# Kernel tuning notes

Hardware: AMD Instinct MI355X
Metric: run time of the kernel (lower is better)

Reference implementation:

```python
import jax, jax.numpy as jnp
import numpy as np

H = 16
D_HEAD = 64  # model_dim // head_count = 1024 // 16
MODEL_DIM = 1024
MODEL_DIM1 = 768


def setup_inputs() -> dict:
    key = jax.random.key(0)
    ks = jax.random.split(key, 12)
    B, Q, K = 4, 1024, 1024
    inp = {
        "key": jax.random.normal(ks[0], (B, K, MODEL_DIM), jnp.float32),
        "value": jax.random.normal(ks[1], (B, K, MODEL_DIM), jnp.float32),
        "query": jax.random.normal(ks[2], (B, Q, MODEL_DIM1), jnp.float32),
        "mask": jax.random.randint(ks[3], (B, Q), 0, 2, jnp.int32),
        "additional_mask": jax.random.randint(ks[4], (B, K), 0, 2, jnp.int32),
        # learned params (nn.Linear weights stored as [in, out] for x @ W)
        "Wk": 0.02 * jax.random.normal(ks[5], (MODEL_DIM, H * D_HEAD), jnp.float32),
        "bk": jnp.zeros((H * D_HEAD,), jnp.float32),
        "Wv": 0.02 * jax.random.normal(ks[6], (MODEL_DIM, H * D_HEAD), jnp.float32),
        "bv": jnp.zeros((H * D_HEAD,), jnp.float32),
        "Wq": 0.02 * jax.random.normal(ks[7], (MODEL_DIM1, H * D_HEAD), jnp.float32),
        "bq": jnp.zeros((H * D_HEAD,), jnp.float32),
        "Wo": 0.02 * jax.random.normal(ks[8], (H * D_HEAD, MODEL_DIM1), jnp.float32),
        "bo": jnp.zeros((MODEL_DIM1,), jnp.float32),
    }
    return inp


def reference(key, value, query, mask, additional_mask, Wk, bk, Wv, bv, Wq, bq, Wo, bo):
    B, K_len = key.shape[0], key.shape[1]
    Q_len = query.shape[1]

    def shape(x):  # [B, L, H*d] -> [B, H, L, d]
        return x.reshape(B, -1, H, D_HEAD).transpose(0, 2, 1, 3)

    k = shape(key @ Wk + bk)
    v = shape(value @ Wv + bv)
    q = shape(query @ Wq + bq) / jnp.sqrt(jnp.float32(D_HEAD))

    scores = jnp.einsum("bhqd,bhkd->bhqk", q, k)  # [B,H,Q,K]
    top_score = scores[:, 0, :, :]  # pre-mask scores of head 0

    neg = jnp.float32(-1e18)
    scores = jnp.where(mask[:, None, :, None] == 0, neg, scores)
    scores = jnp.where(additional_mask[:, None, None, :] == 0, neg, scores)

    attn = jax.nn.softmax(scores, axis=-1)
    # dropout omitted (eval mode / deterministic reference)
    ctx = jnp.einsum("bhqk,bhkd->bhqd", attn, v)
    ctx = ctx.transpose(0, 2, 1, 3).reshape(B, Q_len, H * D_HEAD)
    output = ctx @ Wo + bo
    return output, top_score
```

## Files before the change

kernel.cpp:

```cpp
#include <hip/hip_runtime.h>
#include <hip/hip_bf16.h>

typedef __bf16 bf16_t;
typedef __bf16 bf16x8 __attribute__((ext_vector_type(8)));
typedef __bf16 bf16x4 __attribute__((ext_vector_type(4)));
typedef float  f32x4  __attribute__((ext_vector_type(4)));
typedef int    i32x4  __attribute__((ext_vector_type(4)));

#define MFMA16(a,b,c) __builtin_amdgcn_mfma_f32_16x16x32_bf16((a),(b),(c),0,0,0)

static constexpr int Bn = 4, Hn = 16, Dh = 64, SEQ = 1024;

__device__ __forceinline__ void gll16(const void* g, void* l) {
    __builtin_amdgcn_global_load_lds(
        (const __attribute__((address_space(1))) void*)g,
        (__attribute__((address_space(3))) void*)l, 16, 0, 0);
}

__global__ __launch_bounds__(256)
void wtrans_kernel(const float* __restrict__ s0, const float* __restrict__ s1,
                   const float* __restrict__ s2, const float* __restrict__ s3,
                   bf16_t* __restrict__ d0, bf16_t* __restrict__ d1,
                   bf16_t* __restrict__ d2, bf16_t* __restrict__ d3)
{
    __shared__ bf16_t tile[64][72];
    const int bid = blockIdx.x, t = threadIdx.x;
    const float* src; bf16_t* dst; int R, C, tr, tc;
    if (bid < 256)      { src = s0; dst = d0; R = 1024; C = 1024; tr = bid >> 4;        tc = bid & 15; }
    else if (bid < 512) { src = s1; dst = d1; R = 1024; C = 1024; tr = (bid-256) >> 4;  tc = (bid-256) & 15; }
    else if (bid < 704) { src = s2; dst = d2; R = 768;  C = 1024; tr = (bid-512) >> 4;  tc = (bid-512) & 15; }
    else                { src = s3; dst = d3; R = 1024; C = 768;  tr = (bid-704) / 12;  tc = (bid-704) % 12; }
    const int r0 = tr * 64, c0 = tc * 64;
    const int lr = t >> 2, lc0 = (t & 3) * 16;
    #pragma unroll
    for (int i = 0; i < 4; i++) {
        f32x4 v = *(const f32x4*)&src[(size_t)(r0 + lr) * C + c0 + lc0 + i * 4];
        #pragma unroll
        for (int j = 0; j < 4; j++) tile[lr][lc0 + i * 4 + j] = (bf16_t)v[j];
    }
    __syncthreads();
    const int oc = t >> 2, orc0 = (t & 3) * 16;
    #pragma unroll
    for (int i = 0; i < 2; i++) {
        bf16x8 vv;
        #pragma unroll
        for (int j = 0; j < 8; j++) vv[j] = tile[orc0 + i * 8 + j][oc];
        *(bf16x8*)&dst[(size_t)(c0 + oc) * R + r0 + orc0 + i * 8] = vv;
    }
}

template<int KD, int N, int MODE, typename AT>
__global__ __launch_bounds__(256)
void gemm_bt(const AT* __restrict__ A, const bf16_t* __restrict__ Bt,
             const float* __restrict__ bias, void* __restrict__ outp,
             float scale)
{
    __shared__ bf16_t As[2][128 * 32];
    __shared__ bf16_t Bs[2][64 * 32];
    __shared__ bf16_t Ct[(MODE == 2) ? 1 : 128 * 72];
    const int t = threadIdx.x, lane = t & 63, w = t >> 6;
    const int wr = w >> 1, wc = w & 1;
    const int row0 = blockIdx.y * 128, col0 = blockIdx.x * 64;
    const int lrow = lane & 15, lk4 = lane >> 4, lk8 = lk4 * 8;
    const int ar = t >> 1, ac = (t & 1) * 16;

    f32x4 acc[4][2] = {};
    f32x4 a_f[4];

    auto aload = [&](int kk) {
        if constexpr (sizeof(AT) == 4) {
            const float* src = (const float*)A + (size_t)(row0 + ar) * KD + kk + ac;
            a_f[0] = *(const f32x4*)(src);
            a_f[1] = *(const f32x4*)(src + 4);
            a_f[2] = *(const f32x4*)(src + 8);
            a_f[3] = *(const f32x4*)(src + 12);
        }
    };
    auto awrite = [&](int buf) {
        if constexpr (sizeof(AT) == 4) {
            bf16x8 v0, v1;
            #pragma unroll
            for (int j = 0; j < 4; j++) {
                v0[j] = (bf16_t)a_f[0][j]; v0[4 + j] = (bf16_t)a_f[1][j];
                v1[j] = (bf16_t)a_f[2][j]; v1[4 + j] = (bf16_t)a_f[3][j];
            }
            *(bf16x8*)&As[buf][ar * 32 + ac]     = v0;
            *(bf16x8*)&As[buf][ar * 32 + ac + 8] = v1;
        }
    };
    auto astage_gll = [&](int buf, int kk) {
        if constexpr (sizeof(AT) == 2) {
            #pragma unroll
            for (int j = 0; j < 2; j++) {
                const int idx = j * 256 + t;
                const bf16_t* g = (const bf16_t*)A +
                    (size_t)(row0 + (idx >> 2)) * KD + kk + (idx & 3) * 8;
                gll16(g, &As[buf][(j * 256 + w * 64) * 8]);
            }
        }
    };
    auto bstage = [&](int buf, int kk) {
        const bf16_t* g = Bt + (size_t)(col0 + (t >> 2)) * KD + kk + (t & 3) * 8;
        gll16(g, &Bs[buf][w * 512]);
    };

    constexpr int NB = KD / 32;
    if constexpr (sizeof(AT) == 4) { aload(0); awrite(0); }
    else                            astage_gll(0, 0);
    bstage(0, 0);

    for (int s = 0; s < NB; s++) {
        __syncthreads();
        const int cur = s & 1;
        if (s + 1 < NB) {
            bstage(cur ^ 1, (s + 1) * 32);
            if constexpr (sizeof(AT) == 4) aload((s + 1) * 32);
            else                           astage_gll(cur ^ 1, (s + 1) * 32);
        }
        bf16x8 af[4], bfr[2];
        #pragma unroll
        for (int mf = 0; mf < 4; mf++)
            af[mf] = *(const bf16x8*)&As[cur][(wr * 64 + mf * 16 + lrow) * 32 + lk8];
        #pragma unroll
        for (int nf = 0; nf < 2; nf++)
            bfr[nf] = *(const bf16x8*)&Bs[cur][(wc * 32 + nf * 16 + lrow) * 32 + lk8];
        #pragma unroll
        for (int mf = 0; mf < 4; mf++)
            #pragma unroll
            for (int nf = 0; nf < 2; nf++)
                acc[mf][nf] = MFMA16(af[mf], bfr[nf], acc[mf][nf]);
        if (s + 1 < NB) { if constexpr (sizeof(AT) == 4) awrite(cur ^ 1); }
    }

    if constexpr (MODE == 2) {
        #pragma unroll
        for (int mf = 0; mf < 4; mf++)
            #pragma unroll
            for (int nf = 0; nf < 2; nf++) {
                const int gcol = col0 + wc * 32 + nf * 16 + lrow;
                const float bv = bias[gcol];
                #pragma unroll
                for (int r = 0; r < 4; r++) {
                    const int grow = row0 + wr * 64 + mf * 16 + lk4 * 4 + r;
                    ((float*)outp)[(size_t)grow * N + gcol] = (acc[mf][nf][r] + bv) * scale;
                }
            }
    } else {
        __syncthreads();
        #pragma unroll
        for (int mf = 0; mf < 4; mf++)
            #pragma unroll
            for (int nf = 0; nf < 2; nf++) {
                const int lcol = wc * 32 + nf * 16 + lrow;
                const float bv = bias[col0 + lcol];
                #pragma unroll
                for (int r = 0; r < 4; r++)
                    Ct[(wr * 64 + mf * 16 + lk4 * 4 + r) * 72 + lcol] =
                        (bf16_t)((acc[mf][nf][r] + bv) * scale);
            }
        __syncthreads();
        const int h = col0 >> 6, b = row0 >> 10;
        bf16_t* op = (bf16_t*)outp + ((size_t)(b * Hn + h) << 16);
        if constexpr (MODE == 0) {
            #pragma unroll
            for (int j = 0; j < 4; j++) {
                const int sl = j * 32 + (t >> 3), cl0 = (t & 7) * 8;
                bf16x8 v = *(const bf16x8*)&Ct[sl * 72 + cl0];
                *(bf16x8*)&op[(size_t)((row0 & 1023) + sl) * 64 + cl0] = v;
            }
        } else {
            #pragma unroll
            for (int jj = 0; jj < 2; jj++) {
                const int cl = jj * 32 + (t >> 3);
                #pragma unroll
                for (int k = 0; k < 2; k++) {
                    const int sl0 = k * 64 + (t & 7) * 8;
                    bf16x8 v;
                    #pragma unroll
                    for (int i = 0; i < 8; i++) v[i] = Ct[(sl0 + i) * 72 + cl];
                    *(bf16x8*)&op[(size_t)cl * 1024 + (row0 & 1023) + sl0] = v;
                }
            }
        }
    }
}

__global__ __launch_bounds__(256)
void attn_kernel(const bf16_t* __restrict__ kbuf, const bf16_t* __restrict__ vT,
                 const bf16_t* __restrict__ qbuf, const int* __restrict__ qmask,
                 const int* __restrict__ kmask, bf16_t* __restrict__ ctx)
{
    __shared__ bf16_t Pall[4][16 * 64];
    const int t = threadIdx.x, lane = t & 63, w = t >> 6;
    const int bidx = blockIdx.x;
    const int qt = bidx & 15, bh = bidx >> 4, b = bh >> 4, h = bh & 15;
    const int lrow = lane & 15, lk4 = lane >> 4, lk8 = lk4 * 8;
    const int wrow0 = qt * 64 + w * 16;
    const bf16_t* kb = kbuf + (size_t)bh * SEQ * Dh;
    const bf16_t* vb = vT + (size_t)bh * Dh * SEQ;
    char* Pw = (char*)&Pall[w][0];
    const int sw = (lrow & 7) << 4;

    bf16x8 aq0, aq1;
    {
        const bf16_t* qp = qbuf + ((size_t)bh * SEQ + wrow0 + lrow) * Dh + lk8;
        aq0 = *(const bf16x8*)(qp);
        aq1 = *(const bf16x8*)(qp + 32);
    }
    const int qm = qmask[b * SEQ + wrow0 + lrow];

    float m_run = -__builtin_inff(), l_run = 0.f;
    f32x4 o[4] = {};

    bf16x8 kc0[4], kc1[4];
    #pragma unroll
    for (int nf = 0; nf < 4; nf++) {
        const bf16_t* kp = kb + (size_t)(nf * 16 + lrow) * Dh + lk8;
        kc0[nf] = *(const bf16x8*)(kp);
        kc1[nf] = *(const bf16x8*)(kp + 32);
    }

    for (int kt = 0; kt < 16; kt++) {
        const int key0 = kt * 64;
        bf16x8 vf0[4], vf1[4];
        #pragma unroll
        for (int nf = 0; nf < 4; nf++) {
            const bf16_t* vp = vb + (size_t)(nf * 16 + lrow) * SEQ + key0 + lk8;
            vf0[nf] = *(const bf16x8*)(vp);
            vf1[nf] = *(const bf16x8*)(vp + 32);
        }
        i32x4 km[4];
        #pragma unroll
        for (int nf = 0; nf < 4; nf++)
            km[nf] = *(const i32x4*)&kmask[b * SEQ + key0 + nf * 16 + lk4 * 4];
        f32x4 s4[4] = {};
        #pragma unroll
        for (int nf = 0; nf < 4; nf++) {
            s4[nf] = MFMA16(kc0[nf], aq0, s4[nf]);
            s4[nf] = MFMA16(kc1[nf], aq1, s4[nf]);
        }
        bf16x8 kn0[4], kn1[4];
        if (kt < 15) {
            #pragma unroll
            for (int nf = 0; nf < 4; nf++) {
                const bf16_t* kp = kb + (size_t)(key0 + 64 + nf * 16 + lrow) * Dh + lk8;
                kn0[nf] = *(const bf16x8*)(kp);
                kn1[nf] = *(const bf16x8*)(kp + 32);
            }
        }
        float p[4][4];
        float mt = m_run;
        #pragma unroll
        for (int nf = 0; nf < 4; nf++)
            #pragma unroll
            for (int r = 0; r < 4; r++) {
                const float sv = (qm && km[nf][r]) ? s4[nf][r] : -1e18f;
                p[nf][r] = sv;
                mt = fmaxf(mt, sv);
            }
        mt = fmaxf(mt, __shfl_xor(mt, 16));
        mt = fmaxf(mt, __shfl_xor(mt, 32));
        const float resc = __expf(m_run - mt);
        m_run = mt;
        float rs = 0.f;
        #pragma unroll
        for (int nf = 0; nf < 4; nf++)
            #pragma unroll
            for (int r = 0; r < 4; r++) {
                p[nf][r] = __expf(p[nf][r] - m_run);
                rs += p[nf][r];
            }
        rs += __shfl_xor(rs, 16);
        rs += __shfl_xor(rs, 32);
        l_run = l_run * resc + rs;
        #pragma unroll
        for (int nf = 0; nf < 4; nf++)
            #pragma unroll
            for (int r = 0; r < 4; r++) o[nf][r] *= resc;
        #pragma unroll
        for (int nf = 0; nf < 4; nf++) {
            bf16x4 pk;
            #pragma unroll
            for (int r = 0; r < 4; r++) pk[r] = (bf16_t)p[nf][r];
            *(bf16x4*)(Pw + lrow * 128 + ((nf * 32 + lk4 * 8) ^ sw)) = pk;
        }
        bf16x8 pa0 = *(const bf16x8*)(Pw + lrow * 128 + ((lk4 * 16) ^ sw));
        bf16x8 pa1 = *(const bf16x8*)(Pw + lrow * 128 + ((64 + lk4 * 16) ^ sw));
        #pragma unroll
        for (int nf = 0; nf < 4; nf++) {
            o[nf] = MFMA16(vf0[nf], pa0, o[nf]);
            o[nf] = MFMA16(vf1[nf], pa1, o[nf]);
        }
        #pragma unroll
        for (int nf = 0; nf < 4; nf++) { kc0[nf] = kn0[nf]; kc1[nf] = kn1[nf]; }
    }
    const float inv = 1.0f / l_run;
    #pragma unroll
    for (int nf = 0; nf < 4; nf++) {
        bf16x4 pk;
        #pragma unroll
        for (int r = 0; r < 4; r++) pk[r] = (bf16_t)(o[nf][r] * inv);
        *(bf16x4*)(Pw + lrow * 128 + ((nf * 32 + lk4 * 8) ^ sw)) = pk;
    }
    const int qp2 = lane >> 2, ch = lane & 3;
    const int sw2 = (qp2 & 7) << 4;
    bf16x8 o0 = *(const bf16x8*)(Pw + qp2 * 128 + ((ch * 32) ^ sw2));
    bf16x8 o1 = *(const bf16x8*)(Pw + qp2 * 128 + ((ch * 32 + 16) ^ sw2));
    bf16_t* cp = ctx + ((size_t)(b * SEQ + wrow0 + qp2)) * 1024 + h * 64 + ch * 16;
    *(bf16x8*)cp = o0;
    *(bf16x8*)(cp + 8) = o1;
}

__global__ __launch_bounds__(256)
void topsc_kernel(const bf16_t* __restrict__ kbuf, const bf16_t* __restrict__ qbuf,
                  float* __restrict__ topsc)
{
    const int t = threadIdx.x, lane = t & 63, w = t >> 6;
    const int bx = blockIdx.x;
    const int b = bx >> 6, qt = (bx >> 2) & 15, kq = bx & 3;
    const int lrow = lane & 15, lk4 = lane >> 4, lk8 = lk4 * 8;
    const int wrow0 = qt * 64 + w * 16;
    const bf16_t* kb = kbuf + ((size_t)(b * Hn)) * SEQ * Dh;
    const bf16_t* qp = qbuf + ((size_t)(b * Hn)) * SEQ * Dh
                     + (size_t)(wrow0 + lrow) * Dh + lk8;
    bf16x8 aq0 = *(const bf16x8*)(qp);
    bf16x8 aq1 = *(const bf16x8*)(qp + 32);
    for (int kt = 0; kt < 4; kt++) {
        const int key0 = kq * 256 + kt * 64;
        f32x4 s4[4] = {};
        #pragma unroll
        for (int nf = 0; nf < 4; nf++) {
            const bf16_t* kp = kb + (size_t)(key0 + nf * 16 + lrow) * Dh + lk8;
            s4[nf] = MFMA16(aq0, *(const bf16x8*)(kp), s4[nf]);
            s4[nf] = MFMA16(aq1, *(const bf16x8*)(kp + 32), s4[nf]);
        }
        #pragma unroll
        for (int nf = 0; nf < 4; nf++)
            #pragma unroll
            for (int r = 0; r < 4; r++)
                topsc[(size_t)(b * SEQ + wrow0 + lk4 * 4 + r) * SEQ +
                      key0 + nf * 16 + lrow] = s4[nf][r];
    }
}

extern "C" void kernel_launch(void* const* d_in, const int* in_sizes, int n_in,
                              void* d_out, int out_size, void* d_ws, size_t ws_size,
                              hipStream_t stream)
{
    const float* key   = (const float*)d_in[0];
    const float* value = (const float*)d_in[1];
    const float* query = (const float*)d_in[2];
    const int*   mask  = (const int*)d_in[3];
    const int*   amask = (const int*)d_in[4];
    const float* Wk = (const float*)d_in[5];
    const float* bk = (const float*)d_in[6];
    const float* Wv = (const float*)d_in[7];
    const float* bv = (const float*)d_in[8];
    const float* Wq = (const float*)d_in[9];
    const float* bq = (const float*)d_in[10];
    const float* Wo = (const float*)d_in[11];
    const float* bo = (const float*)d_in[12];

    const size_t per = (size_t)Bn * Hn * SEQ * Dh;
    bf16_t* kproj = (bf16_t*)d_ws;
    bf16_t* vT    = kproj + per;
    bf16_t* qproj = vT + per;
    bf16_t* ctx   = qproj + per;

    float* outf = (float*)d_out;
    bf16_t* WkT = (bf16_t*)(outf + (size_t)Bn * SEQ * 768);
    bf16_t* WvT = WkT + 1024 * 1024;
    bf16_t* WqT = WvT + 1024 * 1024;
    bf16_t* WoT = WqT + 1024 * 768;
    float* topsc = outf + (size_t)Bn * SEQ * 768;

    wtrans_kernel<<<896, 256, 0, stream>>>(Wk, Wv, Wq, Wo, WkT, WvT, WqT, WoT);
    gemm_bt<1024, 1024, 0, float><<<dim3(16, 32), 256, 0, stream>>>(key,   WkT, bk, kproj, 1.0f);
    gemm_bt<1024, 1024, 1, float><<<dim3(16, 32), 256, 0, stream>>>(value, WvT, bv, vT,    1.0f);
    gemm_bt< 768, 1024, 0, float><<<dim3(16, 32), 256, 0, stream>>>(query, WqT, bq, qproj, 0.125f);
    attn_kernel<<<dim3(Bn * Hn * 16), 256, 0, stream>>>(kproj, vT, qproj, mask, amask, ctx);
    gemm_bt<1024, 768, 2, bf16_t><<<dim3(12, 32), 256, 0, stream>>>(ctx, WoT, bo, outf, 1.0f);
    topsc_kernel<<<256, 256, 0, stream>>>(kproj, qproj, topsc);
}
```

Before: 369.2 us.

## Widen GEMM K-step with swizzled LDS; lazy rescale and MFMA row-sum in attention

The projection GEMM now stages 64-wide K slices instead of 32, using an XOR-swizzled LDS layout, so there are half as many barrier iterations and fewer bank conflicts. The attention kernel skips the online-softmax rescale unless the running max grows by more than a threshold. It also computes the row sum with an extra MFMA against a ones vector instead of shuffle reductions, and raises wave priority around MFMA blocks. This uses more LDS and registers and may lower occupancy, and the bf16 row sum adds some rounding error.

```diff
diff --git a/kernel.cpp b/kernel.cpp
--- a/kernel.cpp
+++ b/kernel.cpp
@@ -55,80 +55,102 @@
              const float* __restrict__ bias, void* __restrict__ outp,
              float scale)
 {
-    __shared__ bf16_t As[2][128 * 32];
-    __shared__ bf16_t Bs[2][64 * 32];
+    __shared__ bf16_t As[2][128 * 64];
+    __shared__ bf16_t Bs[2][64 * 64];
     __shared__ bf16_t Ct[(MODE == 2) ? 1 : 128 * 72];
     const int t = threadIdx.x, lane = t & 63, w = t >> 6;
     const int wr = w >> 1, wc = w & 1;
     const int row0 = blockIdx.y * 128, col0 = blockIdx.x * 64;
     const int lrow = lane & 15, lk4 = lane >> 4, lk8 = lk4 * 8;
-    const int ar = t >> 1, ac = (t & 1) * 16;
+    const int ar = t >> 1, ac0 = (t & 1) * 32;
 
     f32x4 acc[4][2] = {};
-    f32x4 a_f[4];
+    f32x4 a_f[8];
 
     auto aload = [&](int kk) {
         if constexpr (sizeof(AT) == 4) {
-            const float* src = (const float*)A + (size_t)(row0 + ar) * KD + kk + ac;
-            a_f[0] = *(const f32x4*)(src);
-            a_f[1] = *(const f32x4*)(src + 4);
-            a_f[2] = *(const f32x4*)(src + 8);
-            a_f[3] = *(const f32x4*)(src + 12);
+            const float* src = (const float*)A + (size_t)(row0 + ar) * KD + kk + ac0;
+            #pragma unroll
+            for (int j = 0; j < 8; j++) a_f[j] = *(const f32x4*)(src + j * 4);
         }
     };
     auto awrite = [&](int buf) {
         if constexpr (sizeof(AT) == 4) {
-            bf16x8 v0, v1;
+            char* base = (char*)&As[buf][0] + ar * 128;
+            const int aswz = (ar & 7) << 4;
             #pragma unroll
             for (int j = 0; j < 4; j++) {
-                v0[j] = (bf16_t)a_f[0][j]; v0[4 + j] = (bf16_t)a_f[1][j];
-                v1[j] = (bf16_t)a_f[2][j]; v1[4 + j] = (bf16_t)a_f[3][j];
-            }
-            *(bf16x8*)&As[buf][ar * 32 + ac]     = v0;
-            *(bf16x8*)&As[buf][ar * 32 + ac + 8] = v1;
+                bf16x8 v;
+                #pragma unroll
+                for (int e = 0; e < 4; e++) {
+                    v[e]     = (bf16_t)a_f[2 * j][e];
+                    v[4 + e] = (bf16_t)a_f[2 * j + 1][e];
+                }
+                *(bf16x8*)(base + ((ac0 * 2 + j * 16) ^ aswz)) = v;
+            }
         }
     };
     auto astage_gll = [&](int buf, int kk) {
         if constexpr (sizeof(AT) == 2) {
             #pragma unroll
-            for (int j = 0; j < 2; j++) {
+            for (int j = 0; j < 4; j++) {
                 const int idx = j * 256 + t;
-                const bf16_t* g = (const bf16_t*)A +
-                    (size_t)(row0 + (idx >> 2)) * KD + kk + (idx & 3) * 8;
-                gll16(g, &As[buf][(j * 256 + w * 64) * 8]);
+                const int row = idx >> 3, colb = (idx & 7) * 16;
+                const bf16_t* g = (const bf16_t*)A + (size_t)(row0 + row) * KD +
+                                  kk + ((colb ^ ((row & 7) << 4)) >> 1);
+                gll16(g, (char*)&As[buf][0] + (j * 256 + w * 64) * 16);
             }
         }
     };
     auto bstage = [&](int buf, int kk) {
-        const bf16_t* g = Bt + (size_t)(col0 + (t >> 2)) * KD + kk + (t & 3) * 8;
-        gll16(g, &Bs[buf][w * 512]);
+        #pragma unroll
+        for (int j = 0; j < 2; j++) {
+            const int idx = j * 256 + t;
+            const int n = idx >> 3, colb = (idx & 7) * 16;
+            const bf16_t* g = Bt + (size_t)(col0 + n) * KD +
+                              kk + ((colb ^ ((n & 7) << 4)) >> 1);
+            gll16(g, (char*)&Bs[buf][0] + (j * 256 + w * 64) * 16);
+        }
     };
 
-    constexpr int NB = KD / 32;
+    constexpr int NB = KD / 64;
     if constexpr (sizeof(AT) == 4) { aload(0); awrite(0); }
     else                            astage_gll(0, 0);
     bstage(0, 0);
 
+    const char* AsC0 = (const char*)&As[0][0];
+    const char* BsC0 = (const char*)&Bs[0][0];
     for (int s = 0; s < NB; s++) {
         __syncthreads();
         const int cur = s & 1;
         if (s + 1 < NB) {
-            bstage(cur ^ 1, (s + 1) * 32);
-            if constexpr (sizeof(AT) == 4) aload((s + 1) * 32);
-            else                           astage_gll(cur ^ 1, (s + 1) * 32);
-        }
-        bf16x8 af[4], bfr[2];
-        #pragma unroll
-        for (int mf = 0; mf < 4; mf++)
-            af[mf] = *(const bf16x8*)&As[cur][(wr * 64 + mf * 16 + lrow) * 32 + lk8];
-        #pragma unroll
-        for (int nf = 0; nf < 2; nf++)
-            bfr[nf] = *(const bf16x8*)&Bs[cur][(wc * 32 + nf * 16 + lrow) * 32 + lk8];
-        #pragma unroll
-        for (int mf = 0; mf < 4; mf++)
-            #pragma unroll
-            for (int nf = 0; nf < 2; nf++)
-                acc[mf][nf] = MFMA16(af[mf], bfr[nf], acc[mf][nf]);
+            bstage(cur ^ 1, (s + 1) * 64);
+            if constexpr (sizeof(AT) == 4) aload((s + 1) * 64);
+            else                           astage_gll(cur ^ 1, (s + 1) * 64);
+        }
+        const char* AsC = AsC0 + cur * (128 * 128);
+        const char* BsC = BsC0 + cur * (64 * 128);
+        #pragma unroll
+        for (int h = 0; h < 2; h++) {
+            bf16x8 af[4], bfr[2];
+            #pragma unroll
+            for (int mf = 0; mf < 4; mf++) {
+                const int R = wr * 64 + mf * 16 + lrow;
+                af[mf] = *(const bf16x8*)(AsC + R * 128 +
+                          (((h * 32 + lk8) * 2) ^ ((R & 7) << 4)));
+            }
+            #pragma unroll
+            for (int nf = 0; nf < 2; nf++) {
+                const int Rn = wc * 32 + nf * 16 + lrow;
+                bfr[nf] = *(const bf16x8*)(BsC + Rn * 128 +
+                          (((h * 32 + lk8) * 2) ^ ((Rn & 7) << 4)));
+            }
+            #pragma unroll
+            for (int mf = 0; mf < 4; mf++)
+                #pragma unroll
+                for (int nf = 0; nf < 2; nf++)
+                    acc[mf][nf] = MFMA16(af[mf], bfr[nf], acc[mf][nf]);
+        }
         if (s + 1 < NB) { if constexpr (sizeof(AT) == 4) awrite(cur ^ 1); }
     }
 
@@ -209,8 +231,13 @@
     }
     const int qm = qmask[b * SEQ + wrow0 + lrow];
 
-    float m_run = -__builtin_inff(), l_run = 0.f;
+    bf16x8 ones;
+    #pragma unroll
+    for (int i = 0; i < 8; i++) ones[i] = (bf16_t)1.0f;
+
+    float m_run = -__builtin_inff();
     f32x4 o[4] = {};
+    f32x4 o_l  = {};
 
     bf16x8 kc0[4], kc1[4];
     #pragma unroll
@@ -234,11 +261,13 @@
         for (int nf = 0; nf < 4; nf++)
             km[nf] = *(const i32x4*)&kmask[b * SEQ + key0 + nf * 16 + lk4 * 4];
         f32x4 s4[4] = {};
+        __builtin_amdgcn_s_setprio(1);
         #pragma unroll
         for (int nf = 0; nf < 4; nf++) {
             s4[nf] = MFMA16(kc0[nf], aq0, s4[nf]);
             s4[nf] = MFMA16(kc1[nf], aq1, s4[nf]);
         }
+        __builtin_amdgcn_s_setprio(0);
         bf16x8 kn0[4], kn1[4];
         if (kt < 15) {
             #pragma unroll
@@ -248,35 +277,31 @@
                 kn1[nf] = *(const bf16x8*)(kp + 32);
             }
         }
-        float p[4][4];
-        float mt = m_run;
+        float p[4][4], mx[4];
+        #pragma unroll
+        for (int nf = 0; nf < 4; nf++) {
+            #pragma unroll
+            for (int r = 0; r < 4; r++)
+                p[nf][r] = (qm && km[nf][r]) ? s4[nf][r] : -1e18f;
+            mx[nf] = fmaxf(fmaxf(p[nf][0], p[nf][1]), fmaxf(p[nf][2], p[nf][3]));
+        }
+        const float pmax = fmaxf(fmaxf(mx[0], mx[1]), fmaxf(mx[2], mx[3]));
+        if (!__all(pmax - m_run <= 8.0f)) {
+            float mt = fmaxf(pmax, __shfl_xor(pmax, 16));
+            mt = fmaxf(mt, __shfl_xor(mt, 32));
+            const float resc = __expf(m_run - mt);
+            m_run = mt;
+            #pragma unroll
+            for (int nf = 0; nf < 4; nf++)
+                #pragma unroll
+                for (int r = 0; r < 4; r++) o[nf][r] *= resc;
+            #pragma unroll
+            for (int r = 0; r < 4; r++) o_l[r] *= resc;
+        }
         #pragma unroll
         for (int nf = 0; nf < 4; nf++)
             #pragma unroll
-            for (int r = 0; r < 4; r++) {
-                const float sv = (qm && km[nf][r]) ? s4[nf][r] : -1e18f;
-                p[nf][r] = sv;
-                mt = fmaxf(mt, sv);
-            }
-        mt = fmaxf(mt, __shfl_xor(mt, 16));
-        mt = fmaxf(mt, __shfl_xor(mt, 32));
-        const float resc = __expf(m_run - mt);
-        m_run = mt;
-        float rs = 0.f;
-        #pragma unroll
-        for (int nf = 0; nf < 4; nf++)
-            #pragma unroll
-            for (int r = 0; r < 4; r++) {
-                p[nf][r] = __expf(p[nf][r] - m_run);
-                rs += p[nf][r];
-            }
-        rs += __shfl_xor(rs, 16);
-        rs += __shfl_xor(rs, 32);
-        l_run = l_run * resc + rs;
-        #pragma unroll
-        for (int nf = 0; nf < 4; nf++)
-            #pragma unroll
-            for (int r = 0; r < 4; r++) o[nf][r] *= resc;
+            for (int r = 0; r < 4; r++) p[nf][r] = __expf(p[nf][r] - m_run);
         #pragma unroll
         for (int nf = 0; nf < 4; nf++) {
             bf16x4 pk;
@@ -286,15 +311,19 @@
         }
         bf16x8 pa0 = *(const bf16x8*)(Pw + lrow * 128 + ((lk4 * 16) ^ sw));
         bf16x8 pa1 = *(const bf16x8*)(Pw + lrow * 128 + ((64 + lk4 * 16) ^ sw));
+        __builtin_amdgcn_s_setprio(1);
         #pragma unroll
         for (int nf = 0; nf < 4; nf++) {
             o[nf] = MFMA16(vf0[nf], pa0, o[nf]);
             o[nf] = MFMA16(vf1[nf], pa1, o[nf]);
         }
+        o_l = MFMA16(ones, pa0, o_l);
+        o_l = MFMA16(ones, pa1, o_l);
+        __builtin_amdgcn_s_setprio(0);
         #pragma unroll
         for (int nf = 0; nf < 4; nf++) { kc0[nf] = kn0[nf]; kc1[nf] = kn1[nf]; }
     }
-    const float inv = 1.0f / l_run;
+    const float inv = 1.0f / o_l[0];
     #pragma unroll
     for (int nf = 0; nf < 4; nf++) {
         bf16x4 pk;
```

After: 382.9 us. 1.04x slower.
